# Performance work log

Hardware: AMD Instinct MI355X
Metric: run time of the kernel (lower is better)

Reference implementation:

```python
import jax, jax.numpy as jnp
import numpy as np

EMBED = 1024
HEAD = 64

def setup_inputs() -> dict:
    key = jax.random.key(0)
    kx, kk, kq, kv = jax.random.split(key, 4)
    x = jax.random.normal(kx, (8, 2048, EMBED), dtype=jnp.float32)
    s = (1.0 / np.sqrt(EMBED)).astype(np.float32) if isinstance(np.sqrt(EMBED), np.ndarray) else np.float32(1.0 / np.sqrt(EMBED))
    # weights stored as [embed, head] so projection is x @ W (equivalent to torch Linear, no bias)
    Wk = jax.random.normal(kk, (EMBED, HEAD), dtype=jnp.float32) * np.float32(EMBED ** -0.5)
    Wq = jax.random.normal(kq, (EMBED, HEAD), dtype=jnp.float32) * np.float32(EMBED ** -0.5)
    Wv = jax.random.normal(kv, (EMBED, HEAD), dtype=jnp.float32) * np.float32(EMBED ** -0.5)
    return {"x": x, "Wk": Wk, "Wq": Wq, "Wv": Wv}

def reference(x, Wk, Wq, Wv):
    B, S, E = x.shape
    k = jnp.einsum('bse,eh->bsh', x, Wk)
    q = jnp.einsum('bse,eh->bsh', x, Wq)
    v = jnp.einsum('bse,eh->bsh', x, Wv)
    # NOTE: original scales by embedding_dim**-0.5, not head_size**-0.5
    scores = jnp.einsum('bqh,bkh->bqk', q, k) * jnp.asarray(E, x.dtype) ** -0.5
    causal = jnp.tril(jnp.ones((S, S), dtype=bool))
    scores = jnp.where(causal, scores, jnp.asarray(-jnp.inf, x.dtype))
    weights = jax.nn.softmax(scores, axis=-1)
    # dropout is identity in eval / p=0
    return jnp.einsum('bqk,bkh->bqh', weights, v)
```

## Files before the change

kernel.cpp:

```cpp
#include <hip/hip_runtime.h>
#include <hip/hip_bf16.h>

typedef __attribute__((ext_vector_type(4))) float f32x4;
typedef __attribute__((ext_vector_type(4))) short s16x4;
typedef __attribute__((ext_vector_type(8))) short s16x8;
typedef __attribute__((ext_vector_type(4))) unsigned short u16x4;

#define MFMA16(a, b, c) __builtin_amdgcn_mfma_f32_16x16x16bf16_1k((a), (b), (c), 0, 0, 0)
#define LOG2E 1.44269504088896340736f
#define NEG_M_L2E (-8.0f * LOG2E)

static __device__ __forceinline__ short f2bf(float f) {
  union { float f; unsigned u; } v; v.f = f;
  unsigned r = v.u + 0x7fffu + ((v.u >> 16) & 1u);
  return (short)(r >> 16);
}
static __device__ __forceinline__ s16x4 vlo(s16x8 v) { return __builtin_shufflevector(v, v, 0, 1, 2, 3); }
static __device__ __forceinline__ s16x4 vhi(s16x8 v) { return __builtin_shufflevector(v, v, 4, 5, 6, 7); }
static __device__ __forceinline__ s16x8 pack8(f32x4 u, f32x4 v) {
  s16x8 r;
  r[0] = f2bf(u[0]); r[1] = f2bf(u[1]); r[2] = f2bf(u[2]); r[3] = f2bf(u[3]);
  r[4] = f2bf(v[0]); r[5] = f2bf(v[1]); r[6] = f2bf(v[2]); r[7] = f2bf(v[3]);
  return r;
}


__global__ __launch_bounds__(256) void wt_kernel(const float* __restrict__ Wq,
                                                 const float* __restrict__ Wk,
                                                 const float* __restrict__ Wv,
                                                 s16x8* __restrict__ wtf) {
  const int sid = blockIdx.x * 256 + threadIdx.x;
  const int lane = sid & 63;
  const int pj = (sid >> 6) % 6;
  const int ks = (sid >> 6) / 6;
  const int l15 = lane & 15, g = lane >> 4;
  s16x8 o;
#pragma unroll
  for (int e = 0; e < 8; e++) {
    const int jj = 2 * pj + (e >> 2);
    const int kk = ks * 16 + 4 * g + (e & 3);
    const int col = (jj & 3) * 16 + l15;
    const float* W = (jj < 4) ? Wq : (jj < 8 ? Wk : Wv);
    const float scl = (jj < 4) ? 0.03125f : 1.0f;
    o[e] = f2bf(W[kk * 64 + col] * scl);
  }
  wtf[sid] = o;
}

__global__ __launch_bounds__(512) void proj_kernel(const float* __restrict__ x,
                                                   const s16x8* __restrict__ wtf,
                                                   s16x8* __restrict__ qf,
                                                   s16x8* __restrict__ kf,
                                                   s16x8* __restrict__ vf) {
  __shared__ char ldsmem[3][40960];
  const int wid = threadIdx.x >> 6;
  const int lane = threadIdx.x & 63;
  const int l15 = lane & 15, g = lane >> 4;
  const int mt = wid & 3, nh = wid >> 2;
  const int tok0 = blockIdx.x * 64;

  const char* xbytes = (const char*)x;
  const char* wbytes = (const char*)wtf;

  f32x4 acc[6];
#pragma unroll
  for (int i = 0; i < 6; i++) acc[i] = (f32x4){0.f, 0.f, 0.f, 0.f};

#define STAGE(buf, kstep)                                                                \
  {                                                                                      \
    const int ks_ = (kstep);                                                             \
    char* const base_ = ldsmem[buf];                                                     \
    _Pragma("unroll")                                                                    \
    for (int i = 0; i < 2; i++) {                                                        \
      const int gb = wid * 128 + i * 64;                                                 \
      const int tok = (gb >> 4) + g;                                                     \
      const char* src = xbytes + (size_t)(tok0 + tok) * 4096 + ks_ * 256 +               \
                        ((size_t)(l15 ^ (tok & 15))) * 16;                               \
      __builtin_amdgcn_global_load_lds((const unsigned*)src,                             \
                                       (unsigned*)(base_ + gb * 16), 16, 0, 0);          \
    }                                                                                    \
    _Pragma("unroll")                                                                    \
    for (int i = 0; i < 3; i++) {                                                        \
      const int gw = wid * 192 + i * 64;                                                 \
      const char* src = wbytes + ((size_t)ks_ * 1536 + gw + lane) * 16;                  \
      __builtin_amdgcn_global_load_lds((const unsigned*)src,                             \
                                       (unsigned*)(base_ + 16384 + gw * 16), 16, 0, 0);  \
    }                                                                                    \
  }

  STAGE(0, 0);
  STAGE(1, 1);

  int curbuf = 0, stgbuf = 2;
  for (int t = 0; t < 16; t++) {
    if (t < 15) {
      asm volatile("s_waitcnt vmcnt(5)" ::: "memory");
    } else {
      asm volatile("s_waitcnt vmcnt(0)" ::: "memory");
    }
    __builtin_amdgcn_s_barrier();
    if (t + 2 < 16) STAGE(stgbuf, t + 2);
    const char* xb = ldsmem[curbuf];
    const char* wb = xb + 16384;
    const int tok = mt * 16 + l15;
    if (nh == 0) {
#pragma unroll
      for (int ks = 0; ks < 4; ks++) {
        const f32x4 xf = *(const f32x4*)(xb + ((size_t)tok * 16 + (((ks * 4 + g) ^ l15))) * 16);
        s16x4 a;
        a[0] = f2bf(xf[0]); a[1] = f2bf(xf[1]); a[2] = f2bf(xf[2]); a[3] = f2bf(xf[3]);
        const s16x8 w0 = *(const s16x8*)(wb + ((size_t)(ks * 6 + 0) * 64 + lane) * 16);
        const s16x8 w1 = *(const s16x8*)(wb + ((size_t)(ks * 6 + 1) * 64 + lane) * 16);
        const s16x8 w2 = *(const s16x8*)(wb + ((size_t)(ks * 6 + 2) * 64 + lane) * 16);
        acc[0] = MFMA16(vlo(w0), a, acc[0]);
        acc[1] = MFMA16(vhi(w0), a, acc[1]);
        acc[2] = MFMA16(vlo(w1), a, acc[2]);
        acc[3] = MFMA16(vhi(w1), a, acc[3]);
        acc[4] = MFMA16(vlo(w2), a, acc[4]);
        acc[5] = MFMA16(vhi(w2), a, acc[5]);
      }
    } else {
#pragma unroll
      for (int ks = 0; ks < 4; ks++) {
        const f32x4 xf = *(const f32x4*)(xb + ((size_t)tok * 16 + (((ks * 4 + g) ^ l15))) * 16);
        s16x4 a;
        a[0] = f2bf(xf[0]); a[1] = f2bf(xf[1]); a[2] = f2bf(xf[2]); a[3] = f2bf(xf[3]);
        const s16x8 w3 = *(const s16x8*)(wb + ((size_t)(ks * 6 + 3) * 64 + lane) * 16);
        const s16x8 w4 = *(const s16x8*)(wb + ((size_t)(ks * 6 + 4) * 64 + lane) * 16);
        const s16x8 w5 = *(const s16x8*)(wb + ((size_t)(ks * 6 + 5) * 64 + lane) * 16);
        acc[0] = MFMA16(vlo(w3), a, acc[0]);
        acc[1] = MFMA16(vhi(w3), a, acc[1]);
        acc[2] = MFMA16(a, vlo(w4), acc[2]);
        acc[3] = MFMA16(a, vhi(w4), acc[3]);
        acc[4] = MFMA16(a, vlo(w5), acc[4]);
        acc[5] = MFMA16(a, vhi(w5), acc[5]);
      }
    }
    curbuf = (curbuf == 2) ? 0 : curbuf + 1;
    stgbuf = (stgbuf == 2) ? 0 : stgbuf + 1;
  }
#undef STAGE

  const int gtile = blockIdx.x * 4 + mt;
  const size_t s0 = (size_t)gtile * 128 + lane;
  if (nh == 0) {
    qf[s0] = pack8(acc[0], acc[1]);
    qf[s0 + 64] = pack8(acc[2], acc[3]);
    kf[s0] = pack8(acc[4], acc[5]);
  } else {
    kf[s0 + 64] = pack8(acc[0], acc[1]);
    vf[s0] = pack8(acc[2], acc[3]);
    vf[s0 + 64] = pack8(acc[4], acc[5]);
  }
}

__global__ __launch_bounds__(256) void attn_kernel(const s16x8* __restrict__ qf,
                                                   const s16x8* __restrict__ kf,
                                                   const s16x8* __restrict__ vf,
                                                   float* __restrict__ out) {
  __shared__ s16x8 stage[4][2][256];
  const int wid = threadIdx.x >> 6;
  const int lane = threadIdx.x & 63;
  const int l15 = lane & 15, g = lane >> 4;
  const int b = blockIdx.x & 7;
  const int t = 127 - (blockIdx.x >> 3);
  const int T = t + 1;
  const int qs = (T + 3) >> 2;
  const int kb = min(wid * qs, T);
  const int ke = min(kb + qs, T);

  const s16x8* qp = qf + (size_t)b * 128 * 128;
  const char* kbytes = (const char*)(kf + (size_t)b * 128 * 128);
  const char* vbytes = (const char*)(vf + (size_t)b * 128 * 128);

  const s16x8 q01 = qp[(size_t)t * 128 + lane];
  const s16x8 q23 = qp[(size_t)t * 128 + 64 + lane];

  f32x4 ot[4];
#pragma unroll
  for (int i = 0; i < 4; i++) ot[i] = (f32x4){0.f, 0.f, 0.f, 0.f};
  float psum = 0.f;

#define AST(buf, tile)                                                                  \
  {                                                                                     \
    const size_t toff = (size_t)(tile) * 2048 + (size_t)lane * 16;                      \
    unsigned* const dst_ = (unsigned*)&stage[wid][buf][0];                              \
    __builtin_amdgcn_global_load_lds((const unsigned*)(kbytes + toff), dst_, 16, 0, 0); \
    __builtin_amdgcn_global_load_lds((const unsigned*)(kbytes + toff + 1024),           \
                                     (unsigned*)((char*)dst_ + 1024), 16, 0, 0);        \
    __builtin_amdgcn_global_load_lds((const unsigned*)(vbytes + toff),                  \
                                     (unsigned*)((char*)dst_ + 2048), 16, 0, 0);        \
    __builtin_amdgcn_global_load_lds((const unsigned*)(vbytes + toff + 1024),           \
                                     (unsigned*)((char*)dst_ + 3072), 16, 0, 0);        \
  }

  if (kb < ke) {
    AST(0, kb);
    int cur = 0;
    for (int tile = kb; tile < ke; ++tile) {
      if (tile + 1 < ke) {
        AST(cur ^ 1, tile + 1);
        asm volatile("s_waitcnt vmcnt(4)" ::: "memory");
      } else {
        asm volatile("s_waitcnt vmcnt(0)" ::: "memory");
      }
      const s16x8* sb = &stage[wid][cur][0];
      const s16x8 kA = sb[lane];
      const s16x8 kB = sb[64 + lane];
      const s16x8 vA = sb[128 + lane];
      const s16x8 vB = sb[192 + lane];
      f32x4 st = (f32x4){0.f, 0.f, 0.f, 0.f};
      st = MFMA16(vlo(kA), vlo(q01), st);
      st = MFMA16(vhi(kA), vhi(q01), st);
      st = MFMA16(vlo(kB), vlo(q23), st);
      st = MFMA16(vhi(kB), vhi(q23), st);
      if (tile == t) {
#pragma unroll
        for (int r = 0; r < 4; r++)
          if (4 * g + r > l15) st[r] = -1e30f;
      }
      s16x4 pf;
#pragma unroll
      for (int r = 0; r < 4; r++) {
        const float p = exp2f(st[r] * LOG2E + NEG_M_L2E);
        psum += p;
        pf[r] = f2bf(p);
      }
      ot[0] = MFMA16(vlo(vA), pf, ot[0]);
      ot[1] = MFMA16(vhi(vA), pf, ot[1]);
      ot[2] = MFMA16(vlo(vB), pf, ot[2]);
      ot[3] = MFMA16(vhi(vB), pf, ot[3]);
      cur ^= 1;
    }
  }
#undef AST

  psum += __shfl_xor(psum, 16);
  psum += __shfl_xor(psum, 32);

  __syncthreads();
  float* const red = (float*)&stage[0][0][0];
  {
    const int base = (wid * 64 + lane) * 17;
#pragma unroll
    for (int dt = 0; dt < 4; dt++)
#pragma unroll
      for (int r = 0; r < 4; r++) red[base + dt * 4 + r] = ot[dt][r];
    red[base + 16] = psum;
  }
  __syncthreads();
  if (wid == 0) {
    float o[16];
#pragma unroll
    for (int j = 0; j < 16; j++) o[j] = 0.f;
    float lt = 0.f;
#pragma unroll
    for (int w = 0; w < 4; w++) {
      const float* src = red + (w * 64 + lane) * 17;
      lt += src[16];
#pragma unroll
      for (int j = 0; j < 16; j++) o[j] += src[j];
    }
    const float inv = 1.0f / lt;
    float* ob = out + (size_t)(b * 128 + t) * 1024 + l15 * 64;
#pragma unroll
    for (int dt = 0; dt < 4; dt++) {
      f32x4 v;
#pragma unroll
      for (int r = 0; r < 4; r++) v[r] = o[dt * 4 + r] * inv;
      *(f32x4*)(ob + dt * 16 + 4 * g) = v;
    }
  }
}

extern "C" void kernel_launch(void* const* d_in, const int* in_sizes, int n_in,
                              void* d_out, int out_size, void* d_ws, size_t ws_size,
                              hipStream_t stream) {
  const float* x = (const float*)d_in[0];
  const float* Wk = (const float*)d_in[1];
  const float* Wq = (const float*)d_in[2];
  const float* Wv = (const float*)d_in[3];
  float* out = (float*)d_out;

  char* ws = (char*)d_ws;
  s16x8* wtf = (s16x8*)ws;
  s16x8* qfb = (s16x8*)(ws + 393216);
  s16x8* kfb = (s16x8*)(ws + 2490368);
  s16x8* vfb = (s16x8*)(ws + 4587520);

  wt_kernel<<<96, 256, 0, stream>>>(Wq, Wk, Wv, wtf);
  proj_kernel<<<256, 512, 0, stream>>>(x, wtf, qfb, kfb, vfb);
  attn_kernel<<<1024, 256, 0, stream>>>(qfb, kfb, vfb, out);
}
```

Measured before the change: 42.97 us.

## Load projection weights directly into registers, shrink LDS to x-only staging

Weight fragments for the QKV projection now go straight from global memory into double-buffered registers, one set prefetched per k-step, instead of being staged through LDS. LDS per block shrinks from about 120KB to 48KB and the launch bound asks for two blocks per CU, which should raise occupancy and cut LDS traffic. The cost is more VGPRs for the weight buffers and more global load instructions per wave, and the vmcnt accounting now has to match the new mix of register loads and LDS-targeted loads.

```diff
diff --git a/kernel.cpp b/kernel.cpp
--- a/kernel.cpp
+++ b/kernel.cpp
@@ -47,12 +47,12 @@
   wtf[sid] = o;
 }
 
-__global__ __launch_bounds__(512) void proj_kernel(const float* __restrict__ x,
-                                                   const s16x8* __restrict__ wtf,
-                                                   s16x8* __restrict__ qf,
-                                                   s16x8* __restrict__ kf,
-                                                   s16x8* __restrict__ vf) {
-  __shared__ char ldsmem[3][40960];
+__global__ __launch_bounds__(512, 2) void proj_kernel(const float* __restrict__ x,
+                                                      const s16x8* __restrict__ wtf,
+                                                      s16x8* __restrict__ qf,
+                                                      s16x8* __restrict__ kf,
+                                                      s16x8* __restrict__ vf) {
+  __shared__ char ldsmem[3][16384];
   const int wid = threadIdx.x >> 6;
   const int lane = threadIdx.x & 63;
   const int l15 = lane & 15, g = lane >> 4;
@@ -60,13 +60,14 @@
   const int tok0 = blockIdx.x * 64;
 
   const char* xbytes = (const char*)x;
-  const char* wbytes = (const char*)wtf;
 
   f32x4 acc[6];
 #pragma unroll
   for (int i = 0; i < 6; i++) acc[i] = (f32x4){0.f, 0.f, 0.f, 0.f};
 
-#define STAGE(buf, kstep)                                                                \
+  s16x8 wreg[2][12];
+
+#define XSTG(buf, kstep)                                                                 \
   {                                                                                      \
     const int ks_ = (kstep);                                                             \
     char* const base_ = ldsmem[buf];                                                     \
@@ -79,39 +80,47 @@
       __builtin_amdgcn_global_load_lds((const unsigned*)src,                             \
                                        (unsigned*)(base_ + gb * 16), 16, 0, 0);          \
     }                                                                                    \
+  }
+
+#define WLOAD(seti, kstep)                                                               \
+  {                                                                                      \
     _Pragma("unroll")                                                                    \
-    for (int i = 0; i < 3; i++) {                                                        \
-      const int gw = wid * 192 + i * 64;                                                 \
-      const char* src = wbytes + ((size_t)ks_ * 1536 + gw + lane) * 16;                  \
-      __builtin_amdgcn_global_load_lds((const unsigned*)src,                             \
-                                       (unsigned*)(base_ + 16384 + gw * 16), 16, 0, 0);  \
-    }                                                                                    \
-  }
-
-  STAGE(0, 0);
-  STAGE(1, 1);
-
-  int curbuf = 0, stgbuf = 2;
+    for (int ks = 0; ks < 4; ks++)                                                       \
+      _Pragma("unroll")                                                                  \
+      for (int i = 0; i < 3; i++)                                                        \
+        wreg[seti][ks * 3 + i] =                                                         \
+            wtf[((size_t)((kstep) * 4 + ks) * 6 + nh * 3 + i) * 64 + lane];              \
+  }
+
+  WLOAD(0, 0);
+  __builtin_amdgcn_sched_barrier(0);
+  XSTG(0, 0);
+  XSTG(1, 1);
+
+#pragma unroll
   for (int t = 0; t < 16; t++) {
     if (t < 15) {
-      asm volatile("s_waitcnt vmcnt(5)" ::: "memory");
+      asm volatile("s_waitcnt vmcnt(2)" ::: "memory");
     } else {
       asm volatile("s_waitcnt vmcnt(0)" ::: "memory");
     }
     __builtin_amdgcn_s_barrier();
-    if (t + 2 < 16) STAGE(stgbuf, t + 2);
-    const char* xb = ldsmem[curbuf];
-    const char* wb = xb + 16384;
+    if (t + 1 < 16) WLOAD((t + 1) & 1, t + 1);
+    __builtin_amdgcn_sched_barrier(0);
+    if (t + 2 < 16) XSTG((t + 2) % 3, t + 2);
+
+    const char* xb = ldsmem[t % 3];
     const int tok = mt * 16 + l15;
+    const s16x8* wr = wreg[t & 1];
     if (nh == 0) {
 #pragma unroll
       for (int ks = 0; ks < 4; ks++) {
         const f32x4 xf = *(const f32x4*)(xb + ((size_t)tok * 16 + (((ks * 4 + g) ^ l15))) * 16);
         s16x4 a;
         a[0] = f2bf(xf[0]); a[1] = f2bf(xf[1]); a[2] = f2bf(xf[2]); a[3] = f2bf(xf[3]);
-        const s16x8 w0 = *(const s16x8*)(wb + ((size_t)(ks * 6 + 0) * 64 + lane) * 16);
-        const s16x8 w1 = *(const s16x8*)(wb + ((size_t)(ks * 6 + 1) * 64 + lane) * 16);
-        const s16x8 w2 = *(const s16x8*)(wb + ((size_t)(ks * 6 + 2) * 64 + lane) * 16);
+        const s16x8 w0 = wr[ks * 3 + 0];
+        const s16x8 w1 = wr[ks * 3 + 1];
+        const s16x8 w2 = wr[ks * 3 + 2];
         acc[0] = MFMA16(vlo(w0), a, acc[0]);
         acc[1] = MFMA16(vhi(w0), a, acc[1]);
         acc[2] = MFMA16(vlo(w1), a, acc[2]);
@@ -125,9 +134,9 @@
         const f32x4 xf = *(const f32x4*)(xb + ((size_t)tok * 16 + (((ks * 4 + g) ^ l15))) * 16);
         s16x4 a;
         a[0] = f2bf(xf[0]); a[1] = f2bf(xf[1]); a[2] = f2bf(xf[2]); a[3] = f2bf(xf[3]);
-        const s16x8 w3 = *(const s16x8*)(wb + ((size_t)(ks * 6 + 3) * 64 + lane) * 16);
-        const s16x8 w4 = *(const s16x8*)(wb + ((size_t)(ks * 6 + 4) * 64 + lane) * 16);
-        const s16x8 w5 = *(const s16x8*)(wb + ((size_t)(ks * 6 + 5) * 64 + lane) * 16);
+        const s16x8 w3 = wr[ks * 3 + 0];
+        const s16x8 w4 = wr[ks * 3 + 1];
+        const s16x8 w5 = wr[ks * 3 + 2];
         acc[0] = MFMA16(vlo(w3), a, acc[0]);
         acc[1] = MFMA16(vhi(w3), a, acc[1]);
         acc[2] = MFMA16(a, vlo(w4), acc[2]);
@@ -136,10 +145,9 @@
         acc[5] = MFMA16(a, vhi(w5), acc[5]);
       }
     }
-    curbuf = (curbuf == 2) ? 0 : curbuf + 1;
-    stgbuf = (stgbuf == 2) ? 0 : stgbuf + 1;
-  }
-#undef STAGE
+  }
+#undef XSTG
+#undef WLOAD
 
   const int gtile = blockIdx.x * 4 + mt;
   const size_t s0 = (size_t)gtile * 128 + lane;
```

Result: slower. 49.07 us (+14.2%).
